# Optimization experiments

Measured on AMD Instinct MI355X. Metric: run time of the kernel, lower is better.

## Reference

```python
import jax, jax.numpy as jnp
import numpy as np

NUM_HEADS = 32
NUM_KV_HEADS = 8
HEAD_DIM = 128
HIDDEN = 4096
B, L = 2, 4096


def _phi(x):
    # feature map: elu(x) + 1
    return jax.nn.elu(x) + 1.0


def setup_inputs() -> dict:
    key = jax.random.key(0)
    ks = jax.random.split(key, 9)
    s = 1.0 / np.sqrt(HIDDEN)
    return {
        "hidden_states": jax.random.normal(ks[0], (B, L, HIDDEN), jnp.float32),
        "Wq": jax.random.normal(ks[1], (HIDDEN, HIDDEN), jnp.float32) * s,
        "bq": jnp.zeros((HIDDEN,), jnp.float32),
        "Wk": jax.random.normal(ks[2], (NUM_KV_HEADS * HEAD_DIM, HIDDEN), jnp.float32) * s,
        "bk": jnp.zeros((NUM_KV_HEADS * HEAD_DIM,), jnp.float32),
        "Wv": jax.random.normal(ks[3], (NUM_KV_HEADS * HEAD_DIM, HIDDEN), jnp.float32) * s,
        "bv": jnp.zeros((NUM_KV_HEADS * HEAD_DIM,), jnp.float32),
        "Wo": jax.random.normal(ks[4], (HIDDEN, HIDDEN), jnp.float32) * s,
        "bo": jnp.zeros((HIDDEN,), jnp.float32),
    }


def reference(hidden_states, Wq, bq, Wk, bk, Wv, bv, Wo, bo):
    bsz, q_len, _ = hidden_states.shape
    n_rep = NUM_HEADS // NUM_KV_HEADS

    # projections (nn.Linear: y = x @ W.T + b)
    q = hidden_states @ Wq.T + bq          # [B, L, H*D]
    k = hidden_states @ Wk.T + bk          # [B, L, Hkv*D]
    v = hidden_states @ Wv.T + bv

    q = q.reshape(bsz, q_len, NUM_HEADS, HEAD_DIM).transpose(0, 2, 1, 3)       # [B,H,L,D]
    k = k.reshape(bsz, q_len, NUM_KV_HEADS, HEAD_DIM).transpose(0, 2, 1, 3)    # [B,Hkv,L,D]
    v = v.reshape(bsz, q_len, NUM_KV_HEADS, HEAD_DIM).transpose(0, 2, 1, 3)

    # repeat_kv: [B,Hkv,L,D] -> [B,H,L,D]
    k = jnp.broadcast_to(k[:, :, None], (bsz, NUM_KV_HEADS, n_rep, q_len, HEAD_DIM)).reshape(bsz, NUM_HEADS, q_len, HEAD_DIM)
    v = jnp.broadcast_to(v[:, :, None], (bsz, NUM_KV_HEADS, n_rep, q_len, HEAD_DIM)).reshape(bsz, NUM_HEADS, q_len, HEAD_DIM)

    q = _phi(q)
    k = _phi(k)

    # global KV summary: O(L*d^2) linear attention
    key_value = jnp.einsum('bhld,bhlv->bhvd', k, v)           # [B,H,D,D]
    attn = jnp.einsum('bhqd,bhvd->bhqv', q, key_value)        # [B,H,L,D]

    # normalizer: sum of feature-mapped keys over sequence, per channel
    normalizer = k.sum(axis=2)[:, :, None, :]                  # [B,H,1,D]
    attn = attn / (normalizer + 1e-10)

    attn = attn.transpose(0, 2, 1, 3).reshape(bsz, q_len, HIDDEN)
    return attn @ Wo.T + bo
```

## Files before the change

kernel.cpp:

```cpp
#include <hip/hip_runtime.h>

#define HIDDEN 4096
#define NKV 8
#define NH 32
#define HD 128
#define BATCH 2
#define SEQ 4096
#define ROWS (BATCH*SEQ)

typedef short bf16x8 __attribute__((ext_vector_type(8)));
typedef float f32x4 __attribute__((ext_vector_type(4)));

static __device__ __forceinline__ float bf2f(unsigned short u) {
    union { unsigned int i; float f; } c; c.i = ((unsigned int)u) << 16; return c.f;
}
static __device__ __forceinline__ unsigned short f2bf(float x) {
    union { float f; unsigned int i; } c; c.f = x;
    unsigned int r = c.i + 0x7fffu + ((c.i >> 16) & 1u);
    return (unsigned short)(r >> 16);
}

static __device__ __forceinline__ void gl2lds16(const void* g, void* l) {
    __builtin_amdgcn_global_load_lds(
        (const __attribute__((address_space(1))) unsigned int*)g,
        (__attribute__((address_space(3))) unsigned int*)l, 16, 0, 0);
}

#define WGBAR() __builtin_amdgcn_s_barrier()
#define VMW(n) asm volatile("s_waitcnt vmcnt(" #n ")" ::: "memory")
#define LGKM(n) asm volatile("s_waitcnt lgkmcnt(" #n ")" ::: "memory")
#define SCHED_FENCE() __builtin_amdgcn_sched_barrier(0)

__global__ __launch_bounds__(256)
void cast_kernel(const float* __restrict__ in, unsigned short* __restrict__ out, int n4) {
    int idx = blockIdx.x * blockDim.x + threadIdx.x;
    int stride = gridDim.x * blockDim.x;
    for (int i = idx; i < n4; i += stride) {
        float4 f = ((const float4*)in)[i];
        ushort4 o;
        o.x = f2bf(f.x); o.y = f2bf(f.y); o.z = f2bf(f.z); o.w = f2bf(f.w);
        ((ushort4*)out)[i] = o;
    }
}

template<int MODE>
__global__ __launch_bounds__(512, 2)
void gemm256(const unsigned short* __restrict__ A, int lda,
             const unsigned short* __restrict__ B, int ldb,
             const float* __restrict__ bias0, const float* __restrict__ bias1,
             void* __restrict__ Cout, int M, int N, int K)
{
    __shared__ __align__(16) unsigned char sm[131072];

    const int tid = threadIdx.x;
    const int wid = tid >> 6, lane = tid & 63;
    const int wr = wid >> 2, wc = wid & 3;
    const int lr = lane & 15, kg = lane >> 4;
    const int swz = (lane & 7) << 4;

    int nbx = N >> 8;
    int nwg = nbx * (M >> 8);
    int cpx = nwg >> 3;
    int bid = (int)blockIdx.x;
    int wg = (bid & 7) * cpx + (bid >> 3);
    int bx = wg % nbx, by = wg / nbx;
    int rowBase = by << 8, colBase = bx << 8;

    size_t sA[2], sB[2];
#pragma unroll
    for (int i = 0; i < 2; ++i) {
        int o = i * 8192 + tid * 16;
        int rm = o >> 7;
        int inner = (o & 127) ^ ((rm & 7) << 4);
        int half = inner >> 6;
        int ke = (inner & 63) >> 1;
        sA[i] = (size_t)(rowBase + half * 128 + rm) * lda + ke;
        sB[i] = (size_t)(colBase + half * 128 + rm) * ldb + ke;
    }
    const int ldsW = wid * 1024;

    auto STAGE = [&](int nb, size_t ko) {
        gl2lds16(A + sA[0] + ko, sm + nb + 0 * 8192 + ldsW);
        gl2lds16(A + sA[1] + ko, sm + nb + 1 * 8192 + ldsW);
        gl2lds16(B + sB[0] + ko, sm + nb + 16384 + 0 * 8192 + ldsW);
        gl2lds16(B + sB[1] + ko, sm + nb + 16384 + 1 * 8192 + ldsW);
    };

    const int aRd = (lr << 7) + ((((wr << 6) | (kg << 4))) ^ swz);
    const int bRd = 16384 + ((((wc & 1) * 64 + lr)) << 7)
                  + (((((wc >> 1) << 6) | (kg << 4))) ^ swz);

    auto RA = [&](int cb, int mp) -> bf16x8 {
        return *(const bf16x8*)(sm + cb + aRd + mp * 2048);
    };
    auto RB = [&](int cb, int n) -> bf16x8 {
        return *(const bf16x8*)(sm + cb + bRd + n * 2048);
    };

    f32x4 acc[8][4] = {};
    bf16x8 bfr[4];

    auto MF2 = [&](bf16x8 x0, bf16x8 x1, int m0, int m1) {
        SCHED_FENCE();
        __builtin_amdgcn_s_setprio(1);
#pragma unroll
        for (int n = 0; n < 4; ++n) {
            acc[m0][n] = __builtin_amdgcn_mfma_f32_16x16x32_bf16(x0, bfr[n], acc[m0][n], 0, 0, 0);
            acc[m1][n] = __builtin_amdgcn_mfma_f32_16x16x32_bf16(x1, bfr[n], acc[m1][n], 0, 0, 0);
        }
        __builtin_amdgcn_s_setprio(0);
        SCHED_FENCE();
    };

    auto TILE = [&](int cb) {
        bfr[0] = RB(cb, 0); bfr[1] = RB(cb, 1); bfr[2] = RB(cb, 2); bfr[3] = RB(cb, 3);
        bf16x8 a0 = RA(cb, 0), a1 = RA(cb, 1);
        SCHED_FENCE();
        bf16x8 a2 = RA(cb, 2), a3 = RA(cb, 3);
        SCHED_FENCE();
        LGKM(2);
        MF2(a0, a1, 0, 1);
        a0 = RA(cb, 4); a1 = RA(cb, 5);
        SCHED_FENCE();
        LGKM(2);
        MF2(a2, a3, 2, 3);
        a2 = RA(cb, 6); a3 = RA(cb, 7);
        SCHED_FENCE();
        LGKM(2);
        MF2(a0, a1, 4, 5);
        LGKM(0);
        MF2(a2, a3, 6, 7);
    };

    const int NT = K >> 5;

    SCHED_FENCE();
    STAGE(0, 0);
    STAGE(32768, 32);
    SCHED_FENCE();
    VMW(4);
    WGBAR();
    SCHED_FENCE();

    int cur = 0;
    size_t ko = 64;
    for (int t = 0; t < NT - 2; ++t) {
        const int cb = cur << 15;
        const int nb = ((cur + 2) & 3) << 15;
        SCHED_FENCE();
        STAGE(nb, ko);
        SCHED_FENCE();
        TILE(cb);
        VMW(4);
        WGBAR();
        SCHED_FENCE();
        cur = (cur + 1) & 3; ko += 32;
    }
    {
        const int cb = cur << 15;
        TILE(cb);
        VMW(0);
        WGBAR();
        SCHED_FENCE();
        cur = (cur + 1) & 3;
    }
    {
        const int cb = cur << 15;
        TILE(cb);
    }

    int r0 = rowBase + wr * 128 + kg * 4;
    int c0 = colBase + wc * 64 + lr;
#pragma unroll
    for (int n = 0; n < 4; ++n) {
        int col = c0 + n * 16;
        float bv;
        if (MODE == 2) bv = (col < 1024) ? bias0[col] : bias1[col - 1024];
        else           bv = bias0[col];
#pragma unroll
        for (int m = 0; m < 8; ++m) {
            int row = r0 + m * 16;
#pragma unroll
            for (int r = 0; r < 4; ++r) {
                float v = acc[m][n][r] + bv;
                if (MODE == 1) v = (v > 0.f) ? v + 1.f : __expf(v);
                if (MODE == 2 && col < 1024) v = (v > 0.f) ? v + 1.f : __expf(v);
                if (MODE == 0) ((float*)Cout)[(size_t)(row + r) * N + col] = v;
                else ((unsigned short*)Cout)[(size_t)(row + r) * N + col] = f2bf(v);
            }
        }
    }
}

__global__ __launch_bounds__(256)
void kv_partial(const unsigned short* __restrict__ Kb, const unsigned short* __restrict__ Vb,
                int ld, float* __restrict__ kvp, float* __restrict__ ksp)
{
    int chunk = blockIdx.x;
    int g = blockIdx.y;
    int b = g >> 3, hkv = g & 7;
    __shared__ float kl[32][128];
    __shared__ float vl[32][128];
    int tid = threadIdx.x;
    int c0 = (tid >> 4) * 8, d0 = (tid & 15) * 8;
    float acc[8][8] = {};
    float ksacc = 0.0f;
    size_t rowBase = (size_t)b * SEQ + (size_t)chunk * 128;

    for (int sch = 0; sch < 4; ++sch) {
        __syncthreads();
        for (int t = tid; t < 512; t += 256) {
            int l = t >> 4, col = (t & 15) * 8;
            size_t off = (rowBase + sch * 32 + l) * ld + hkv * HD + col;
            uint4 kr = *(const uint4*)(Kb + off);
            uint4 vr = *(const uint4*)(Vb + off);
            unsigned int ku[4] = {kr.x, kr.y, kr.z, kr.w};
            unsigned int vu[4] = {vr.x, vr.y, vr.z, vr.w};
#pragma unroll
            for (int q = 0; q < 4; ++q) {
                kl[l][col + q * 2]     = bf2f((unsigned short)(ku[q] & 0xffff));
                kl[l][col + q * 2 + 1] = bf2f((unsigned short)(ku[q] >> 16));
                vl[l][col + q * 2]     = bf2f((unsigned short)(vu[q] & 0xffff));
                vl[l][col + q * 2 + 1] = bf2f((unsigned short)(vu[q] >> 16));
            }
        }
        __syncthreads();
        for (int l = 0; l < 32; ++l) {
            float vv[8], kk[8];
#pragma unroll
            for (int x = 0; x < 8; ++x) { vv[x] = vl[l][c0 + x]; kk[x] = kl[l][d0 + x]; }
#pragma unroll
            for (int x = 0; x < 8; ++x)
#pragma unroll
                for (int y = 0; y < 8; ++y)
                    acc[x][y] += vv[x] * kk[y];
        }
        if (tid < 128) {
            for (int l = 0; l < 32; ++l) ksacc += kl[l][tid];
        }
    }
    float* out = kvp + ((size_t)g * 32 + chunk) * (HD * HD);
#pragma unroll
    for (int x = 0; x < 8; ++x)
#pragma unroll
        for (int y = 0; y < 8; ++y)
            out[(c0 + x) * HD + d0 + y] = acc[x][y];
    if (tid < 128) ksp[((size_t)g * 32 + chunk) * HD + tid] = ksacc;
}

__global__ __launch_bounds__(256)
void kv_reduce(const float* __restrict__ kvp, const float* __restrict__ ksp,
               unsigned short* __restrict__ kvb, float* __restrict__ ksum)
{
    int slice = blockIdx.x;
    int g = blockIdx.y;
    int tid = threadIdx.x;
    int e = slice * 1024 + tid * 4;
    float4 s = {0.f, 0.f, 0.f, 0.f};
    for (int ch = 0; ch < 32; ++ch) {
        float4 p = *(const float4*)(kvp + ((size_t)g * 32 + ch) * (HD * HD) + e);
        s.x += p.x; s.y += p.y; s.z += p.z; s.w += p.w;
    }
    ushort4 o;
    o.x = f2bf(s.x); o.y = f2bf(s.y); o.z = f2bf(s.z); o.w = f2bf(s.w);
    *(ushort4*)(kvb + (size_t)g * HD * HD + e) = o;
    if (slice == 0 && tid < 128) {
        float ss = 0.f;
        for (int ch = 0; ch < 32; ++ch) ss += ksp[((size_t)g * 32 + ch) * HD + tid];
        ksum[g * HD + tid] = ss;
    }
}

__global__ __launch_bounds__(256)
void attn_gemm(const unsigned short* __restrict__ Q,
               const unsigned short* __restrict__ KV,
               const float* __restrict__ KS,
               unsigned short* __restrict__ Out)
{
    const int BK = 32;
    __shared__ unsigned short As[128 * BK];
    __shared__ unsigned short Bs[128 * BK];

    int rt = blockIdx.x;
    int h  = blockIdx.y;
    int g = (rt >> 5) * NKV + (h >> 2);
    int rowBase = rt << 7;

    const unsigned short* A = Q + (size_t)h * HD;
    const unsigned short* B = KV + (size_t)g * HD * HD;
    const float* ks = KS + g * HD;

    int tid = threadIdx.x;
    int wave = tid >> 6, lane = tid & 63;
    int wr = wave >> 1, wc = wave & 1;

    f32x4 acc[4][4] = {};

    int sr = lane >> 2;
    int sc = (lane & 3) * 8;

    const unsigned short* Aw = A + (size_t)(rowBase + wave * 32 + sr) * HIDDEN + sc;
    const unsigned short* Bw = B + (size_t)(wave * 32 + sr) * HD + sc;
    unsigned short* Asw = As + wave * 32 * BK;
    unsigned short* Bsw = Bs + wave * 32 * BK;

    int arow = (wr * 64 + (lane & 15)) * BK + (lane >> 4) * 8;
    int brow = (wc * 64 + (lane & 15)) * BK + (lane >> 4) * 8;

    for (int kt = 0; kt < HD; kt += BK) {
        gl2lds16(Aw + kt, Asw);
        gl2lds16(Aw + kt + (size_t)16 * HIDDEN, Asw + 16 * BK);
        gl2lds16(Bw + kt, Bsw);
        gl2lds16(Bw + kt + (size_t)16 * HD, Bsw + 16 * BK);
        __syncthreads();
        bf16x8 af[4], bfr[4];
#pragma unroll
        for (int i = 0; i < 4; ++i) af[i] = *(const bf16x8*)&As[arow + i * 16 * BK];
#pragma unroll
        for (int j = 0; j < 4; ++j) bfr[j] = *(const bf16x8*)&Bs[brow + j * 16 * BK];
#pragma unroll
        for (int i = 0; i < 4; ++i)
#pragma unroll
            for (int j = 0; j < 4; ++j)
                acc[i][j] = __builtin_amdgcn_mfma_f32_16x16x32_bf16(af[i], bfr[j], acc[i][j], 0, 0, 0);
        __syncthreads();
    }

    int r0 = rowBase + wr * 64 + ((lane >> 4) << 2);
    int c0 = wc * 64 + (lane & 15);
#pragma unroll
    for (int j = 0; j < 4; ++j) {
        int col = c0 + j * 16;
        float inv = 1.0f / (ks[col] + 1e-10f);
#pragma unroll
        for (int i = 0; i < 4; ++i) {
            int row = r0 + i * 16;
#pragma unroll
            for (int r = 0; r < 4; ++r) {
                float v = acc[i][j][r] * inv;
                Out[(size_t)(row + r) * HIDDEN + h * HD + col] = f2bf(v);
            }
        }
    }
}

extern "C" void kernel_launch(void* const* d_in, const int* in_sizes, int n_in,
                              void* d_out, int out_size, void* d_ws, size_t ws_size,
                              hipStream_t stream)
{
    const float* hs = (const float*)d_in[0];
    const float* Wq = (const float*)d_in[1];
    const float* bq = (const float*)d_in[2];
    const float* Wk = (const float*)d_in[3];
    const float* bk = (const float*)d_in[4];
    const float* Wv = (const float*)d_in[5];
    const float* bv = (const float*)d_in[6];
    const float* Wo = (const float*)d_in[7];
    const float* bo = (const float*)d_in[8];

    char* ws = (char*)d_ws;
    size_t off = 0;
    auto alloc = [&](size_t bytes) -> char* {
        char* p = ws + off;
        off += (bytes + 255) & ~(size_t)255;
        return p;
    };

    unsigned short* hs_b  = (unsigned short*)alloc((size_t)ROWS * HIDDEN * 2);
    unsigned short* Wq_b  = (unsigned short*)alloc((size_t)HIDDEN * HIDDEN * 2);
    unsigned short* Wkv_b = (unsigned short*)alloc((size_t)2048 * HIDDEN * 2);
    unsigned short* Wo_b  = (unsigned short*)alloc((size_t)HIDDEN * HIDDEN * 2);
    unsigned short* kvout = (unsigned short*)alloc((size_t)ROWS * 2048 * 2);
    float* ksp   = (float*)alloc((size_t)16 * 32 * HD * 4);
    unsigned short* kvb = (unsigned short*)alloc((size_t)16 * HD * HD * 2);
    float* ksum  = (float*)alloc((size_t)16 * HD * 4);

    float* kvp = (float*)Wq_b;
    unsigned short* attn_b = hs_b;
    unsigned short* q_b = (unsigned short*)d_out;

    (void)in_sizes; (void)n_in; (void)out_size; (void)ws_size;

    auto cast = [&](const float* in, unsigned short* out, size_t n) {
        int n4 = (int)(n / 4);
        int blocks = (n4 + 255) / 256;
        if (blocks > 2048) blocks = 2048;
        cast_kernel<<<dim3(blocks), dim3(256), 0, stream>>>(in, out, n4);
    };

    cast(hs, hs_b, (size_t)ROWS * HIDDEN);
    cast(Wq, Wq_b, (size_t)HIDDEN * HIDDEN);
    cast(Wk, Wkv_b, (size_t)1024 * HIDDEN);
    cast(Wv, Wkv_b + (size_t)1024 * HIDDEN, (size_t)1024 * HIDDEN);
    cast(Wo, Wo_b, (size_t)HIDDEN * HIDDEN);

    gemm256<1><<<dim3(512), dim3(512), 0, stream>>>(hs_b, HIDDEN, Wq_b, HIDDEN, bq, nullptr, q_b, ROWS, HIDDEN, HIDDEN);
    gemm256<2><<<dim3(256), dim3(512), 0, stream>>>(hs_b, HIDDEN, Wkv_b, HIDDEN, bk, bv, kvout, ROWS, 2048, HIDDEN);

    kv_partial<<<dim3(32, 16), dim3(256), 0, stream>>>(kvout, kvout + 1024, 2048, kvp, ksp);
    kv_reduce<<<dim3(16, 16), dim3(256), 0, stream>>>(kvp, ksp, kvb, ksum);

    attn_gemm<<<dim3(64, 32), dim3(256), 0, stream>>>(q_b, kvb, ksum, attn_b);

    gemm256<0><<<dim3(512), dim3(512), 0, stream>>>(attn_b, HIDDEN, Wo_b, HIDDEN, bo, nullptr, d_out, ROWS, HIDDEN, HIDDEN);
}
```

Measured before the change: 796.7 us.

## Software-pipeline LDS fragment reads across tiles in bf16 GEMM main loop

Restructures the GEMM main loop to prefetch the next tile's B fragments and first A fragments from LDS into a second register set while the current tile's MFMAs run. The loop is unrolled by four, with ping-pong register sets and constant buffer offsets. This targets the LDS-read latency at the start of each tile. In exchange it waits for all outstanding global loads (vmcnt 0) every step instead of leaving one stage in flight, which may expose global-load latency. It also hardcodes the trip count for K=4096.

```diff
diff --git a/kernel.cpp b/kernel.cpp
--- a/kernel.cpp
+++ b/kernel.cpp
@@ -28,8 +28,9 @@
 
 #define WGBAR() __builtin_amdgcn_s_barrier()
 #define VMW(n) asm volatile("s_waitcnt vmcnt(" #n ")" ::: "memory")
-#define LGKM(n) asm volatile("s_waitcnt lgkmcnt(" #n ")" ::: "memory")
+#define LGKMS(s) asm volatile("s_waitcnt lgkmcnt(" s ")" ::: "memory")
 #define SCHED_FENCE() __builtin_amdgcn_sched_barrier(0)
+#define MFMA_(a,b,c) __builtin_amdgcn_mfma_f32_16x16x32_bf16((a),(b),(c),0,0,0)
 
 __global__ __launch_bounds__(256)
 void cast_kernel(const float* __restrict__ in, unsigned short* __restrict__ out, int n4) {
@@ -98,76 +99,73 @@
     };
 
     f32x4 acc[8][4] = {};
-    bf16x8 bfr[4];
-
-    auto MF2 = [&](bf16x8 x0, bf16x8 x1, int m0, int m1) {
-        SCHED_FENCE();
-        __builtin_amdgcn_s_setprio(1);
-#pragma unroll
-        for (int n = 0; n < 4; ++n) {
-            acc[m0][n] = __builtin_amdgcn_mfma_f32_16x16x32_bf16(x0, bfr[n], acc[m0][n], 0, 0, 0);
-            acc[m1][n] = __builtin_amdgcn_mfma_f32_16x16x32_bf16(x1, bfr[n], acc[m1][n], 0, 0, 0);
-        }
-        __builtin_amdgcn_s_setprio(0);
-        SCHED_FENCE();
-    };
-
-    auto TILE = [&](int cb) {
-        bfr[0] = RB(cb, 0); bfr[1] = RB(cb, 1); bfr[2] = RB(cb, 2); bfr[3] = RB(cb, 3);
-        bf16x8 a0 = RA(cb, 0), a1 = RA(cb, 1);
-        SCHED_FENCE();
-        bf16x8 a2 = RA(cb, 2), a3 = RA(cb, 3);
-        SCHED_FENCE();
-        LGKM(2);
-        MF2(a0, a1, 0, 1);
-        a0 = RA(cb, 4); a1 = RA(cb, 5);
-        SCHED_FENCE();
-        LGKM(2);
-        MF2(a2, a3, 2, 3);
-        a2 = RA(cb, 6); a3 = RA(cb, 7);
-        SCHED_FENCE();
-        LGKM(2);
-        MF2(a0, a1, 4, 5);
-        LGKM(0);
-        MF2(a2, a3, 6, 7);
-    };
-
-    const int NT = K >> 5;
+
+#define MFC(B0,B1,B2,B3, X0, X1, M0, M1) \
+    { SCHED_FENCE(); \
+      __builtin_amdgcn_s_setprio(1); \
+      acc[M0][0]=MFMA_(X0,B0,acc[M0][0]); acc[M1][0]=MFMA_(X1,B0,acc[M1][0]); \
+      acc[M0][1]=MFMA_(X0,B1,acc[M0][1]); acc[M1][1]=MFMA_(X1,B1,acc[M1][1]); \
+      acc[M0][2]=MFMA_(X0,B2,acc[M0][2]); acc[M1][2]=MFMA_(X1,B2,acc[M1][2]); \
+      acc[M0][3]=MFMA_(X0,B3,acc[M0][3]); acc[M1][3]=MFMA_(X1,B3,acc[M1][3]); \
+      __builtin_amdgcn_s_setprio(0); }
+
+#define TILE_STEP(CB, NB, SB, BC0,BC1,BC2,BC3, AC0, AC1, BN0,BN1,BN2,BN3, AN0, AN1, DO_STAGE, DO_PRE, KO, L2, L3) \
+    { \
+        SCHED_FENCE(); \
+        if (DO_STAGE) { STAGE((SB), (KO)); } \
+        SCHED_FENCE(); \
+        bf16x8 t2a = RA((CB),2), t2b = RA((CB),3); \
+        SCHED_FENCE(); \
+        LGKMS("2");                  \
+        MFC(BC0,BC1,BC2,BC3, AC0, AC1, 0, 1); \
+        bf16x8 t3a = RA((CB),4), t3b = RA((CB),5); \
+        SCHED_FENCE(); \
+        LGKMS("2");                  \
+        MFC(BC0,BC1,BC2,BC3, t2a, t2b, 2, 3); \
+        bf16x8 t4a = RA((CB),6), t4b = RA((CB),7); \
+        SCHED_FENCE(); \
+        if (DO_PRE) { BN0=RB((NB),0); BN1=RB((NB),1); BN2=RB((NB),2); BN3=RB((NB),3); } \
+        SCHED_FENCE(); \
+        LGKMS(L2);                   \
+        MFC(BC0,BC1,BC2,BC3, t3a, t3b, 4, 5); \
+        if (DO_PRE) { AN0 = RA((NB),0); AN1 = RA((NB),1); } \
+        SCHED_FENCE(); \
+        LGKMS(L3);                   \
+        MFC(BC0,BC1,BC2,BC3, t4a, t4b, 6, 7); \
+        VMW(0);                      \
+        WGBAR(); \
+        SCHED_FENCE(); \
+    }
+
+    bf16x8 bX0, bX1, bX2, bX3, aX0, aX1;
+    bf16x8 bY0, bY1, bY2, bY3, aY0, aY1;
 
     SCHED_FENCE();
     STAGE(0, 0);
     STAGE(32768, 32);
     SCHED_FENCE();
-    VMW(4);
+    VMW(0);
     WGBAR();
     SCHED_FENCE();
-
-    int cur = 0;
-    size_t ko = 64;
-    for (int t = 0; t < NT - 2; ++t) {
-        const int cb = cur << 15;
-        const int nb = ((cur + 2) & 3) << 15;
-        SCHED_FENCE();
-        STAGE(nb, ko);
-        SCHED_FENCE();
-        TILE(cb);
-        VMW(4);
-        WGBAR();
-        SCHED_FENCE();
-        cur = (cur + 1) & 3; ko += 32;
-    }
-    {
-        const int cb = cur << 15;
-        TILE(cb);
-        VMW(0);
-        WGBAR();
-        SCHED_FENCE();
-        cur = (cur + 1) & 3;
-    }
-    {
-        const int cb = cur << 15;
-        TILE(cb);
-    }
+    bX0 = RB(0, 0); bX1 = RB(0, 1); bX2 = RB(0, 2); bX3 = RB(0, 3);
+    aX0 = RA(0, 0); aX1 = RA(0, 1);
+    SCHED_FENCE();
+
+    size_t kb = 64;
+    for (int it = 0; it < 31; ++it) {
+        TILE_STEP(0,     32768, 65536, bX0,bX1,bX2,bX3, aX0, aX1, bY0,bY1,bY2,bY3, aY0, aY1, 1, 1, kb,      "6", "6");
+        TILE_STEP(32768, 65536, 98304, bY0,bY1,bY2,bY3, aY0, aY1, bX0,bX1,bX2,bX3, aX0, aX1, 1, 1, kb + 32, "6", "6");
+        TILE_STEP(65536, 98304, 0,     bX0,bX1,bX2,bX3, aX0, aX1, bY0,bY1,bY2,bY3, aY0, aY1, 1, 1, kb + 64, "6", "6");
+        TILE_STEP(98304, 0,     32768, bY0,bY1,bY2,bY3, aY0, aY1, bX0,bX1,bX2,bX3, aX0, aX1, 1, 1, kb + 96, "6", "6");
+        kb += 128;
+    }
+    TILE_STEP(0,     32768, 65536, bX0,bX1,bX2,bX3, aX0, aX1, bY0,bY1,bY2,bY3, aY0, aY1, 1, 1, 4032, "6", "6");
+    TILE_STEP(32768, 65536, 98304, bY0,bY1,bY2,bY3, aY0, aY1, bX0,bX1,bX2,bX3, aX0, aX1, 1, 1, 4064, "6", "6");
+    TILE_STEP(65536, 98304, 0,     bX0,bX1,bX2,bX3, aX0, aX1, bY0,bY1,bY2,bY3, aY0, aY1, 0, 1, 0,    "6", "6");
+    TILE_STEP(98304, 0,     0,     bY0,bY1,bY2,bY3, aY0, aY1, bX0,bX1,bX2,bX3, aX0, aX1, 0, 0, 0,    "2", "0");
+
+#undef TILE_STEP
+#undef MFC
 
     int r0 = rowBase + wr * 128 + kg * 4;
     int c0 = colBase + wc * 64 + lr;
```

New measurement: 856.5 us. +7.5%, slower.
